# Kernel optimization log

Measured on AMD Instinct MI355X. Metric: run time of the kernel, lower is better.

The kernel has to match this reference:

```python
import math
import jax, jax.numpy as jnp
import numpy as np

B, T, C = 4, 2048, 1024

def setup_inputs() -> dict:
    key = jax.random.key(0)
    k1, k2 = jax.random.split(key)
    x = jax.random.normal(k1, (B, T, C), dtype=jnp.float32)
    W_kqv = jax.random.normal(k2, (C, 3 * C), dtype=jnp.float32) * 0.02
    return {"x": x, "W_kqv": W_kqv}

def reference(x, W_kqv):
    Bq, Tq, Cq = x.shape
    qkv = jnp.einsum('btc,cd->btd', x, W_kqv)            # [B,T,3C]
    q, k, v = jnp.split(qkv, 3, axis=2)                   # each [B,T,C]
    # scaled scores: note scale is 1/sqrt(n_embed), matching the source
    attn = jnp.einsum('btc,bsc->bts', q, k) / math.sqrt(Cq)  # [B,T,T]
    mask = jnp.tril(jnp.ones((Tq, Tq), dtype=bool))
    attn = jnp.where(mask, attn, -jnp.inf)
    attn = jax.nn.softmax(attn, axis=-1)
    y = jnp.einsum('bts,bsc->btc', attn, v)               # [B,T,C]
    return y
```

## Files before the change

### kernel.cpp

```cpp
#include <hip/hip_runtime.h>

typedef unsigned short u16;
typedef __bf16 bf16x8 __attribute__((ext_vector_type(8)));
typedef float f32x4 __attribute__((ext_vector_type(4)));

#define Bb 4
#define Tt 2048
#define Cc 1024

#define GLOAD_LDS16(g, l)                                                     \
  __builtin_amdgcn_global_load_lds(                                           \
      (const __attribute__((address_space(1))) void*)(g),                     \
      (__attribute__((address_space(3))) void*)(l), 16, 0, 0)

#define WAITV8 asm volatile("s_waitcnt vmcnt(8)" ::: "memory")
#define WAITV0 asm volatile("s_waitcnt vmcnt(0)" ::: "memory")

__device__ inline u16 f2bf(float f) {
  unsigned u = __builtin_bit_cast(unsigned, f);
  unsigned r = u + 0x7fffu + ((u >> 16) & 1u);
  return (u16)(r >> 16);
}

__global__ __launch_bounds__(256) void cast_f32_bf16_vec4(
    const float* __restrict__ in, u16* __restrict__ out, int n4) {
  int i = blockIdx.x * 256 + threadIdx.x;
  if (i >= n4) return;
  float4 v = reinterpret_cast<const float4*>(in)[i];
  ushort4 o;
  o.x = f2bf(v.x); o.y = f2bf(v.y); o.z = f2bf(v.z); o.w = f2bf(v.w);
  reinterpret_cast<ushort4*>(out)[i] = o;
}

__global__ __launch_bounds__(256) void zero_f32(float* __restrict__ p, int n) {
  int i = blockIdx.x * 256 + threadIdx.x;
  if (i < n) p[i] = 0.f;
}

__global__ __launch_bounds__(256) void transpose_cast_w(
    const float* __restrict__ W, u16* __restrict__ Wt) {
  __shared__ float tile[32][33];
  int n0 = blockIdx.x * 32;
  int k0 = blockIdx.y * 32;
  int tx = threadIdx.x;
  int ty = threadIdx.y;
#pragma unroll
  for (int i = 0; i < 4; i++)
    tile[ty + i * 8][tx] = W[(size_t)(k0 + ty + i * 8) * 3072 + n0 + tx];
  __syncthreads();
#pragma unroll
  for (int i = 0; i < 4; i++)
    Wt[(size_t)(n0 + ty + i * 8) * 1024 + k0 + tx] = f2bf(tile[tx][ty + i * 8]);
}

__device__ __forceinline__ void stage_unit(const u16* __restrict__ G, int ld,
                                           u16* lds_unit, int tid) {
#pragma unroll
  for (int j = 0; j < 2; j++) {
    int u = j * 8192 + tid * 16;
    int l = u ^ (((u >> 7) & 7) << 4);
    GLOAD_LDS16(G + (size_t)(l >> 6) * ld + ((l & 63) >> 1), lds_unit + (u >> 1));
  }
}

__device__ __forceinline__ bf16x8 lds_frag(const u16* unit, int row, int fq) {
  int off = row * 64 + fq * 16;
  off ^= ((off >> 7) & 7) << 4;
  return *reinterpret_cast<const bf16x8*>(
      reinterpret_cast<const char*>(unit) + off);
}

__device__ __forceinline__ void stageA256(const u16* __restrict__ G,
                                          u16* unit, int tid) {
#pragma unroll
  for (int j = 0; j < 4; j++) {
    int u = j * 4096 + tid * 16;
    int l = u ^ (((u >> 7) & 7) << 4);
    GLOAD_LDS16(G + (size_t)(l >> 6) * Cc + ((l & 63) >> 1), unit + (u >> 1));
  }
}
__device__ __forceinline__ void stageB256(const u16* __restrict__ G,
                                          u16* unit, int tid) {
#pragma unroll
  for (int j = 0; j < 2; j++) {
    int u = j * 4096 + tid * 16;
    int l = u ^ (((u >> 7) & 7) << 4);
    GLOAD_LDS16(G + (size_t)(l >> 6) * Cc + ((l & 63) >> 1), unit + (u >> 1));
  }
}

__global__ __launch_bounds__(256, 3) void gemm_qkv_256x128(
    const u16* __restrict__ A0, const u16* __restrict__ B0,
    u16* __restrict__ qO, u16* __restrict__ kO, u16* __restrict__ vTO) {
  const int NT = Cc / 32;
  int bx = blockIdx.x, by = blockIdx.y;
  const u16* A = A0 + (size_t)by * 256 * Cc;
  const u16* Bt = B0 + (size_t)bx * 128 * Cc;

  __shared__ __attribute__((aligned(16))) u16 ldsA[2][8192];
  __shared__ __attribute__((aligned(16))) u16 ldsB[2][4096];

  int tid = threadIdx.x;
  int lane = tid & 63, w = tid >> 6;
  int wm = (w >> 1) * 128, wn = (w & 1) * 64;
  int fr = lane & 15, fq = lane >> 4;

  f32x4 acc[8][4] = {};

  stageA256(A, ldsA[0], tid);
  stageB256(Bt, ldsB[0], tid);
  WAITV0;
  __builtin_amdgcn_s_barrier();

  for (int t = 0; t < NT; ++t) {
    int par = t & 1, parn = par ^ 1;
    if (t + 1 < NT) {
      stageA256(A + (t + 1) * 32, ldsA[parn], tid);
      stageB256(Bt + (t + 1) * 32, ldsB[parn], tid);
    }
    bf16x8 a[4], b[4];
#pragma unroll
    for (int ni = 0; ni < 4; ni++)
      b[ni] = lds_frag(ldsB[par], wn + ni * 16 + fr, fq);
#pragma unroll
    for (int mi = 0; mi < 4; mi++)
      a[mi] = lds_frag(ldsA[par], wm + mi * 16 + fr, fq);
    __builtin_amdgcn_s_setprio(1);
#pragma unroll
    for (int mi = 0; mi < 4; mi++)
#pragma unroll
      for (int ni = 0; ni < 4; ni++)
        acc[mi][ni] = __builtin_amdgcn_mfma_f32_16x16x32_bf16(a[mi], b[ni], acc[mi][ni], 0, 0, 0);
    __builtin_amdgcn_s_setprio(0);
#pragma unroll
    for (int mi = 0; mi < 4; mi++)
      a[mi] = lds_frag(ldsA[par], wm + 64 + mi * 16 + fr, fq);
    __builtin_amdgcn_s_setprio(1);
#pragma unroll
    for (int mi = 0; mi < 4; mi++)
#pragma unroll
      for (int ni = 0; ni < 4; ni++)
        acc[4 + mi][ni] = __builtin_amdgcn_mfma_f32_16x16x32_bf16(a[mi], b[ni], acc[4 + mi][ni], 0, 0, 0);
    __builtin_amdgcn_s_setprio(0);
    if (t + 1 < NT) WAITV0;
    __builtin_amdgcn_s_barrier();
  }

#pragma unroll
  for (int mi = 0; mi < 8; mi++) {
#pragma unroll
    for (int ni = 0; ni < 4; ni++) {
#pragma unroll
      for (int r = 0; r < 4; r++) {
        int m = by * 256 + wm + mi * 16 + fq * 4 + r;
        int n = bx * 128 + wn + ni * 16 + fr;
        u16 hv = f2bf(acc[mi][ni][r]);
        int seg = n >> 10, cn = n & 1023;
        int b = m >> 11, tt = m & 2047;
        if (seg == 0)
          qO[(((size_t)(b * Tt + tt)) << 10) + cn] = hv;
        else if (seg == 1)
          kO[(((size_t)(b * Tt + tt)) << 10) + cn] = hv;
        else
          vTO[((size_t)(b * Cc + cn)) * Tt + tt] = hv;
      }
    }
  }
}

template <int MODE>
__global__ __launch_bounds__(512, 2) void gemm256(
    const u16* __restrict__ A0, const u16* __restrict__ B0,
    size_t sAbatch, size_t sBbatch,
    u16* __restrict__ EO, float* __restrict__ rowsum) {
  const int lda = Cc, ldb = Cc, NT = Cc / 64;
  int bx = blockIdx.x, by = blockIdx.y, bz = blockIdx.z;
  if (MODE == 1 && bx > by) return;

  const u16* A = A0 + (size_t)bz * sAbatch + (size_t)by * 256 * lda;
  const u16* Bt = B0 + (size_t)bz * sBbatch + (size_t)bx * 256 * ldb;

  __shared__ __attribute__((aligned(16))) u16 lds[4][2][8192];

  int tid = threadIdx.x;
  int lane = tid & 63, w = tid >> 6;
  int wm = (w >> 2) * 128, wn = (w & 3) * 64;
  int fr = lane & 15, fq = lane >> 4;

  f32x4 acc[8][4] = {};

  stage_unit(A + 0, lda, &lds[0][0][0], tid);
  stage_unit(Bt + 0, ldb, &lds[2][0][0], tid);
  stage_unit(A + 32, lda, &lds[1][0][0], tid);
  stage_unit(Bt + 32, ldb, &lds[3][0][0], tid);
  stage_unit(A + 64, lda, &lds[0][1][0], tid);
  stage_unit(Bt + 64, ldb, &lds[2][1][0], tid);
  WAITV8;
  __builtin_amdgcn_s_barrier();

  for (int t = 0; t < NT; ++t) {
    int par = t & 1;
    int parn = par ^ 1;
    bool st1 = (t + 1 < NT);
    bool st2 = (t + 2 < NT);
    bool tail = (t >= NT - 2);
    bf16x8 a[4], b[4];

#pragma unroll
    for (int mi = 0; mi < 4; mi++)
      a[mi] = lds_frag(&lds[0][par][0], wm + mi * 16 + fr, fq);
#pragma unroll
    for (int ni = 0; ni < 4; ni++)
      b[ni] = lds_frag(&lds[2][par][0], wn + ni * 16 + fr, fq);
    if (st1) stage_unit(A + (t + 1) * 64 + 32, lda, &lds[1][parn][0], tid);
    __builtin_amdgcn_s_barrier();
    __builtin_amdgcn_s_setprio(1);
#pragma unroll
    for (int mi = 0; mi < 4; mi++)
#pragma unroll
      for (int ni = 0; ni < 4; ni++)
        acc[mi][ni] = __builtin_amdgcn_mfma_f32_16x16x32_bf16(a[mi], b[ni], acc[mi][ni], 0, 0, 0);
    __builtin_amdgcn_s_setprio(0);
    __builtin_amdgcn_s_barrier();

#pragma unroll
    for (int mi = 0; mi < 4; mi++)
      a[mi] = lds_frag(&lds[0][par][0], wm + 64 + mi * 16 + fr, fq);
    if (st1) stage_unit(Bt + (t + 1) * 64 + 32, ldb, &lds[3][parn][0], tid);
    __builtin_amdgcn_s_barrier();
    __builtin_amdgcn_s_setprio(1);
#pragma unroll
    for (int mi = 0; mi < 4; mi++)
#pragma unroll
      for (int ni = 0; ni < 4; ni++)
        acc[4 + mi][ni] = __builtin_amdgcn_mfma_f32_16x16x32_bf16(a[mi], b[ni], acc[4 + mi][ni], 0, 0, 0);
    __builtin_amdgcn_s_setprio(0);
    if (tail) { WAITV0; } else { WAITV8; }
    __builtin_amdgcn_s_barrier();

#pragma unroll
    for (int mi = 0; mi < 4; mi++)
      a[mi] = lds_frag(&lds[1][par][0], wm + mi * 16 + fr, fq);
#pragma unroll
    for (int ni = 0; ni < 4; ni++)
      b[ni] = lds_frag(&lds[3][par][0], wn + ni * 16 + fr, fq);
    if (st2) stage_unit(A + (t + 2) * 64, lda, &lds[0][par][0], tid);
    __builtin_amdgcn_s_barrier();
    __builtin_amdgcn_s_setprio(1);
#pragma unroll
    for (int mi = 0; mi < 4; mi++)
#pragma unroll
      for (int ni = 0; ni < 4; ni++)
        acc[mi][ni] = __builtin_amdgcn_mfma_f32_16x16x32_bf16(a[mi], b[ni], acc[mi][ni], 0, 0, 0);
    __builtin_amdgcn_s_setprio(0);
    __builtin_amdgcn_s_barrier();

#pragma unroll
    for (int mi = 0; mi < 4; mi++)
      a[mi] = lds_frag(&lds[1][par][0], wm + 64 + mi * 16 + fr, fq);
    if (st2) stage_unit(Bt + (t + 2) * 64, ldb, &lds[2][par][0], tid);
    __builtin_amdgcn_s_barrier();
    __builtin_amdgcn_s_setprio(1);
#pragma unroll
    for (int mi = 0; mi < 4; mi++)
#pragma unroll
      for (int ni = 0; ni < 4; ni++)
        acc[4 + mi][ni] = __builtin_amdgcn_mfma_f32_16x16x32_bf16(a[mi], b[ni], acc[4 + mi][ni], 0, 0, 0);
    __builtin_amdgcn_s_setprio(0);
    if (tail) { WAITV0; } else { WAITV8; }
    __builtin_amdgcn_s_barrier();
  }

  {
    float rpart[8][4];
#pragma unroll
    for (int mi = 0; mi < 8; mi++)
#pragma unroll
      for (int r = 0; r < 4; r++) rpart[mi][r] = 0.f;
#pragma unroll
    for (int mi = 0; mi < 8; mi++) {
#pragma unroll
      for (int ni = 0; ni < 4; ni++) {
#pragma unroll
        for (int r = 0; r < 4; r++) {
          int m = by * 256 + wm + mi * 16 + fq * 4 + r;
          int n = bx * 256 + wn + ni * 16 + fr;
          float e = 0.f;
          if (n <= m) e = __expf(fminf(acc[mi][ni][r] * 0.03125f, 30.f));
          EO[((size_t)bz * Tt + m) * Tt + n] = f2bf(e);
          rpart[mi][r] += e;
        }
      }
    }
#pragma unroll
    for (int mi = 0; mi < 8; mi++) {
#pragma unroll
      for (int r = 0; r < 4; r++) {
        float v = rpart[mi][r];
        v += __shfl_xor(v, 1);
        v += __shfl_xor(v, 2);
        v += __shfl_xor(v, 4);
        v += __shfl_xor(v, 8);
        if (fr == 0) {
          int m = by * 256 + wm + mi * 16 + fq * 4 + r;
          atomicAdd(&rowsum[(size_t)bz * Tt + m], v);
        }
      }
    }
  }
}

__global__ __launch_bounds__(256) void gemm_bt_pv(
    const u16* __restrict__ A0, const u16* __restrict__ B0,
    size_t sAbatch, size_t sBbatch,
    int K, int lda, int ldb, const float* __restrict__ rowsum,
    float* __restrict__ YO) {
  int bx = blockIdx.x, by = blockIdx.y, bz = blockIdx.z;

  const u16* A = A0 + (size_t)bz * sAbatch + (size_t)by * 128 * lda;
  const u16* Bt = B0 + (size_t)bz * sBbatch + (size_t)bx * 128 * ldb;
  int kEnd = min(K, (by + 1) * 128);

  __shared__ __attribute__((aligned(16))) u16 As[128 * 32];
  __shared__ __attribute__((aligned(16))) u16 Bs[128 * 32];

  int tid = threadIdx.x;
  int lane = tid & 63, w = tid >> 6;
  int wr = (w >> 1) * 64, wc = (w & 1) * 64;
  int row16 = lane & 15, kq = (lane >> 4) * 8;

  int r0 = w * 16 + (lane >> 2);
  int c0 = (lane & 3) * 8;

  f32x4 acc[4][4] = {};

  for (int kt = 0; kt < kEnd; kt += 32) {
    const u16* Ag = A + (size_t)r0 * lda + kt + c0;
    const u16* Bg = Bt + (size_t)r0 * ldb + kt + c0;
    GLOAD_LDS16(Ag, &As[w * 512]);
    GLOAD_LDS16(Ag + (size_t)64 * lda, &As[2048 + w * 512]);
    GLOAD_LDS16(Bg, &Bs[w * 512]);
    GLOAD_LDS16(Bg + (size_t)64 * ldb, &Bs[2048 + w * 512]);
    __syncthreads();

    bf16x8 a[4], b[4];
#pragma unroll
    for (int m = 0; m < 4; m++)
      a[m] = *reinterpret_cast<const bf16x8*>(&As[(wr + m * 16 + row16) * 32 + kq]);
#pragma unroll
    for (int n = 0; n < 4; n++)
      b[n] = *reinterpret_cast<const bf16x8*>(&Bs[(wc + n * 16 + row16) * 32 + kq]);
#pragma unroll
    for (int m = 0; m < 4; m++)
#pragma unroll
      for (int n = 0; n < 4; n++)
        acc[m][n] = __builtin_amdgcn_mfma_f32_16x16x32_bf16(a[m], b[n], acc[m][n], 0, 0, 0);
    __syncthreads();
  }

  int colf = lane & 15, rbase = (lane >> 4) * 4;
#pragma unroll
  for (int i = 0; i < 4; i++) {
#pragma unroll
    for (int r = 0; r < 4; r++) {
      int m = by * 128 + wr + i * 16 + rbase + r;
      float inv = 1.0f / rowsum[(size_t)bz * Tt + m];
#pragma unroll
      for (int j = 0; j < 4; j++) {
        int n = bx * 128 + wc + j * 16 + colf;
        YO[((size_t)bz * Tt + m) * Cc + n] = acc[i][j][r] * inv;
      }
    }
  }
}

extern "C" void kernel_launch(void* const* d_in, const int* in_sizes, int n_in,
                              void* d_out, int out_size, void* d_ws, size_t ws_size,
                              hipStream_t stream) {
  const float* x = (const float*)d_in[0];
  const float* W = (const float*)d_in[1];
  float* Y = (float*)d_out;

  char* ws = (char*)d_ws;
  size_t off = 0;
  auto carve = [&](size_t bytes) -> void* {
    void* p = ws + off;
    off += (bytes + 255) & ~(size_t)255;
    return p;
  };
  u16* xb = (u16*)carve((size_t)Bb * Tt * Cc * 2);
  u16* wt = (u16*)carve((size_t)3 * Cc * Cc * 2);
  u16* qb = (u16*)carve((size_t)Bb * Tt * Cc * 2);
  u16* kb = (u16*)carve((size_t)Bb * Tt * Cc * 2);
  u16* vT = (u16*)carve((size_t)Bb * Cc * Tt * 2);
  u16* E = (u16*)carve((size_t)Bb * Tt * Tt * 2);
  float* rowsum = (float*)carve((size_t)Bb * Tt * 4);

  cast_f32_bf16_vec4<<<(Bb * Tt * Cc / 4 + 255) / 256, 256, 0, stream>>>(
      x, xb, Bb * Tt * Cc / 4);
  zero_f32<<<(Bb * Tt + 255) / 256, 256, 0, stream>>>(rowsum, Bb * Tt);
  transpose_cast_w<<<dim3(96, 32), dim3(32, 8), 0, stream>>>(W, wt);
  gemm_qkv_256x128<<<dim3(24, 32), 256, 0, stream>>>(xb, wt, qb, kb, vT);
  gemm256<1><<<dim3(8, 8, 4), 512, 0, stream>>>(
      qb, kb, (size_t)Tt * Cc, (size_t)Tt * Cc, E, rowsum);
  gemm_bt_pv<<<dim3(8, 16, 4), 256, 0, stream>>>(
      E, vT, (size_t)Tt * Tt, (size_t)Cc * Tt, Tt, Tt, Tt, rowsum, Y);
}
```

Baseline: 306.7 us.

## Retile QKV GEMM to 256x384 tiles with 8 waves and deeper staged pipeline

The QKV projection GEMM moves from 256x128 tiles with 4 waves and a 2-deep buffer to 256x384 tiles with 8 waves. K steps grow to 64, split into two 32-wide sub-buffers that are prefetched with interleaved barriers and partial vmcnt waits. The grid shrinks to 256 blocks, exactly one per CU, which cuts redundant A loads and raises arithmetic intensity. In exchange, occupancy drops to one block per CU and the accumulator register count grows. The templated score GEMM is de-templated without any change to its behaviour.

```diff
diff --git a/kernel.cpp b/kernel.cpp
--- a/kernel.cpp
+++ b/kernel.cpp
@@ -13,6 +13,7 @@
       (const __attribute__((address_space(1))) void*)(g),                     \
       (__attribute__((address_space(3))) void*)(l), 16, 0, 0)
 
+#define WAITV10 asm volatile("s_waitcnt vmcnt(10)" ::: "memory")
 #define WAITV8 asm volatile("s_waitcnt vmcnt(8)" ::: "memory")
 #define WAITV0 asm volatile("s_waitcnt vmcnt(0)" ::: "memory")
 
@@ -53,13 +54,22 @@
     Wt[(size_t)(n0 + ty + i * 8) * 1024 + k0 + tx] = f2bf(tile[tx][ty + i * 8]);
 }
 
-__device__ __forceinline__ void stage_unit(const u16* __restrict__ G, int ld,
-                                           u16* lds_unit, int tid) {
+__device__ __forceinline__ void stage_unitA(const u16* __restrict__ G,
+                                            u16* lds_unit, int tid) {
 #pragma unroll
   for (int j = 0; j < 2; j++) {
     int u = j * 8192 + tid * 16;
     int l = u ^ (((u >> 7) & 7) << 4);
-    GLOAD_LDS16(G + (size_t)(l >> 6) * ld + ((l & 63) >> 1), lds_unit + (u >> 1));
+    GLOAD_LDS16(G + (size_t)(l >> 6) * Cc + ((l & 63) >> 1), lds_unit + (u >> 1));
+  }
+}
+__device__ __forceinline__ void stage_unitB3(const u16* __restrict__ G,
+                                             u16* lds_unit, int tid) {
+#pragma unroll
+  for (int j = 0; j < 3; j++) {
+    int u = j * 8192 + tid * 16;
+    int l = u ^ (((u >> 7) & 7) << 4);
+    GLOAD_LDS16(G + (size_t)(l >> 6) * Cc + ((l & 63) >> 1), lds_unit + (u >> 1));
   }
 }
 
@@ -70,90 +80,113 @@
       reinterpret_cast<const char*>(unit) + off);
 }
 
-__device__ __forceinline__ void stageA256(const u16* __restrict__ G,
-                                          u16* unit, int tid) {
-#pragma unroll
-  for (int j = 0; j < 4; j++) {
-    int u = j * 4096 + tid * 16;
-    int l = u ^ (((u >> 7) & 7) << 4);
-    GLOAD_LDS16(G + (size_t)(l >> 6) * Cc + ((l & 63) >> 1), unit + (u >> 1));
-  }
-}
-__device__ __forceinline__ void stageB256(const u16* __restrict__ G,
-                                          u16* unit, int tid) {
-#pragma unroll
-  for (int j = 0; j < 2; j++) {
-    int u = j * 4096 + tid * 16;
-    int l = u ^ (((u >> 7) & 7) << 4);
-    GLOAD_LDS16(G + (size_t)(l >> 6) * Cc + ((l & 63) >> 1), unit + (u >> 1));
-  }
-}
-
-__global__ __launch_bounds__(256, 3) void gemm_qkv_256x128(
+__global__ __launch_bounds__(512, 1) void gemm_qkv_384(
     const u16* __restrict__ A0, const u16* __restrict__ B0,
     u16* __restrict__ qO, u16* __restrict__ kO, u16* __restrict__ vTO) {
-  const int NT = Cc / 32;
+  const int NT = Cc / 64;
   int bx = blockIdx.x, by = blockIdx.y;
   const u16* A = A0 + (size_t)by * 256 * Cc;
-  const u16* Bt = B0 + (size_t)bx * 128 * Cc;
-
-  __shared__ __attribute__((aligned(16))) u16 ldsA[2][8192];
-  __shared__ __attribute__((aligned(16))) u16 ldsB[2][4096];
+  const u16* Bt = B0 + (size_t)bx * 384 * Cc;
+
+  __shared__ __attribute__((aligned(16))) u16 ldsA[2][2][8192];
+  __shared__ __attribute__((aligned(16))) u16 ldsB[2][2][12288];
 
   int tid = threadIdx.x;
   int lane = tid & 63, w = tid >> 6;
-  int wm = (w >> 1) * 128, wn = (w & 1) * 64;
+  int wm = (w >> 2) * 128, wn = (w & 3) * 96;
   int fr = lane & 15, fq = lane >> 4;
 
-  f32x4 acc[8][4] = {};
-
-  stageA256(A, ldsA[0], tid);
-  stageB256(Bt, ldsB[0], tid);
-  WAITV0;
+  f32x4 acc[8][6] = {};
+
+  stage_unitA(A + 0, &ldsA[0][0][0], tid);
+  stage_unitB3(Bt + 0, &ldsB[0][0][0], tid);
+  stage_unitA(A + 32, &ldsA[1][0][0], tid);
+  stage_unitB3(Bt + 32, &ldsB[1][0][0], tid);
+  stage_unitA(A + 64, &ldsA[0][1][0], tid);
+  stage_unitB3(Bt + 64, &ldsB[0][1][0], tid);
+  WAITV10;
   __builtin_amdgcn_s_barrier();
 
   for (int t = 0; t < NT; ++t) {
     int par = t & 1, parn = par ^ 1;
-    if (t + 1 < NT) {
-      stageA256(A + (t + 1) * 32, ldsA[parn], tid);
-      stageB256(Bt + (t + 1) * 32, ldsB[parn], tid);
-    }
-    bf16x8 a[4], b[4];
-#pragma unroll
-    for (int ni = 0; ni < 4; ni++)
-      b[ni] = lds_frag(ldsB[par], wn + ni * 16 + fr, fq);
-#pragma unroll
-    for (int mi = 0; mi < 4; mi++)
-      a[mi] = lds_frag(ldsA[par], wm + mi * 16 + fr, fq);
-    __builtin_amdgcn_s_setprio(1);
-#pragma unroll
-    for (int mi = 0; mi < 4; mi++)
-#pragma unroll
-      for (int ni = 0; ni < 4; ni++)
+    bool st1 = (t + 1 < NT);
+    bool st2 = (t + 2 < NT);
+    bool tail = (t >= NT - 2);
+    bf16x8 a[4], b[6];
+
+#pragma unroll
+    for (int mi = 0; mi < 4; mi++)
+      a[mi] = lds_frag(&ldsA[0][par][0], wm + mi * 16 + fr, fq);
+#pragma unroll
+    for (int ni = 0; ni < 6; ni++)
+      b[ni] = lds_frag(&ldsB[0][par][0], wn + ni * 16 + fr, fq);
+    if (st1) stage_unitA(A + (t + 1) * 64 + 32, &ldsA[1][parn][0], tid);
+    __builtin_amdgcn_s_barrier();
+    __builtin_amdgcn_s_setprio(1);
+#pragma unroll
+    for (int mi = 0; mi < 4; mi++)
+#pragma unroll
+      for (int ni = 0; ni < 6; ni++)
         acc[mi][ni] = __builtin_amdgcn_mfma_f32_16x16x32_bf16(a[mi], b[ni], acc[mi][ni], 0, 0, 0);
     __builtin_amdgcn_s_setprio(0);
-#pragma unroll
-    for (int mi = 0; mi < 4; mi++)
-      a[mi] = lds_frag(ldsA[par], wm + 64 + mi * 16 + fr, fq);
-    __builtin_amdgcn_s_setprio(1);
-#pragma unroll
-    for (int mi = 0; mi < 4; mi++)
-#pragma unroll
-      for (int ni = 0; ni < 4; ni++)
+    __builtin_amdgcn_s_barrier();
+
+#pragma unroll
+    for (int mi = 0; mi < 4; mi++)
+      a[mi] = lds_frag(&ldsA[0][par][0], wm + 64 + mi * 16 + fr, fq);
+    if (st1) stage_unitB3(Bt + (t + 1) * 64 + 32, &ldsB[1][parn][0], tid);
+    __builtin_amdgcn_s_barrier();
+    __builtin_amdgcn_s_setprio(1);
+#pragma unroll
+    for (int mi = 0; mi < 4; mi++)
+#pragma unroll
+      for (int ni = 0; ni < 6; ni++)
         acc[4 + mi][ni] = __builtin_amdgcn_mfma_f32_16x16x32_bf16(a[mi], b[ni], acc[4 + mi][ni], 0, 0, 0);
     __builtin_amdgcn_s_setprio(0);
-    if (t + 1 < NT) WAITV0;
+    if (tail) { WAITV0; } else { WAITV10; }
+    __builtin_amdgcn_s_barrier();
+
+#pragma unroll
+    for (int mi = 0; mi < 4; mi++)
+      a[mi] = lds_frag(&ldsA[1][par][0], wm + mi * 16 + fr, fq);
+#pragma unroll
+    for (int ni = 0; ni < 6; ni++)
+      b[ni] = lds_frag(&ldsB[1][par][0], wn + ni * 16 + fr, fq);
+    if (st2) stage_unitA(A + (t + 2) * 64, &ldsA[0][par][0], tid);
+    __builtin_amdgcn_s_barrier();
+    __builtin_amdgcn_s_setprio(1);
+#pragma unroll
+    for (int mi = 0; mi < 4; mi++)
+#pragma unroll
+      for (int ni = 0; ni < 6; ni++)
+        acc[mi][ni] = __builtin_amdgcn_mfma_f32_16x16x32_bf16(a[mi], b[ni], acc[mi][ni], 0, 0, 0);
+    __builtin_amdgcn_s_setprio(0);
+    __builtin_amdgcn_s_barrier();
+
+#pragma unroll
+    for (int mi = 0; mi < 4; mi++)
+      a[mi] = lds_frag(&ldsA[1][par][0], wm + 64 + mi * 16 + fr, fq);
+    if (st2) stage_unitB3(Bt + (t + 2) * 64, &ldsB[0][par][0], tid);
+    __builtin_amdgcn_s_barrier();
+    __builtin_amdgcn_s_setprio(1);
+#pragma unroll
+    for (int mi = 0; mi < 4; mi++)
+#pragma unroll
+      for (int ni = 0; ni < 6; ni++)
+        acc[4 + mi][ni] = __builtin_amdgcn_mfma_f32_16x16x32_bf16(a[mi], b[ni], acc[4 + mi][ni], 0, 0, 0);
+    __builtin_amdgcn_s_setprio(0);
+    if (tail) { WAITV0; } else { WAITV10; }
     __builtin_amdgcn_s_barrier();
   }
 
 #pragma unroll
   for (int mi = 0; mi < 8; mi++) {
 #pragma unroll
-    for (int ni = 0; ni < 4; ni++) {
+    for (int ni = 0; ni < 6; ni++) {
 #pragma unroll
       for (int r = 0; r < 4; r++) {
         int m = by * 256 + wm + mi * 16 + fq * 4 + r;
-        int n = bx * 128 + wn + ni * 16 + fr;
+        int n = bx * 384 + wn + ni * 16 + fr;
         u16 hv = f2bf(acc[mi][ni][r]);
         int seg = n >> 10, cn = n & 1023;
         int b = m >> 11, tt = m & 2047;
@@ -168,14 +201,23 @@
   }
 }
 
-template <int MODE>
-__global__ __launch_bounds__(512, 2) void gemm256(
+__device__ __forceinline__ void stage_unit(const u16* __restrict__ G, int ld,
+                                           u16* lds_unit, int tid) {
+#pragma unroll
+  for (int j = 0; j < 2; j++) {
+    int u = j * 8192 + tid * 16;
+    int l = u ^ (((u >> 7) & 7) << 4);
+    GLOAD_LDS16(G + (size_t)(l >> 6) * ld + ((l & 63) >> 1), lds_unit + (u >> 1));
+  }
+}
+
+__global__ __launch_bounds__(512, 2) void gemm256_e(
     const u16* __restrict__ A0, const u16* __restrict__ B0,
     size_t sAbatch, size_t sBbatch,
     u16* __restrict__ EO, float* __restrict__ rowsum) {
   const int lda = Cc, ldb = Cc, NT = Cc / 64;
   int bx = blockIdx.x, by = blockIdx.y, bz = blockIdx.z;
-  if (MODE == 1 && bx > by) return;
+  if (bx > by) return;
 
   const u16* A = A0 + (size_t)bz * sAbatch + (size_t)by * 256 * lda;
   const u16* Bt = B0 + (size_t)bz * sBbatch + (size_t)bx * 256 * ldb;
@@ -400,8 +442,8 @@
       x, xb, Bb * Tt * Cc / 4);
   zero_f32<<<(Bb * Tt + 255) / 256, 256, 0, stream>>>(rowsum, Bb * Tt);
   transpose_cast_w<<<dim3(96, 32), dim3(32, 8), 0, stream>>>(W, wt);
-  gemm_qkv_256x128<<<dim3(24, 32), 256, 0, stream>>>(xb, wt, qb, kb, vT);
-  gemm256<1><<<dim3(8, 8, 4), 512, 0, stream>>>(
+  gemm_qkv_384<<<dim3(8, 32), 512, 0, stream>>>(xb, wt, qb, kb, vT);
+  gemm256_e<<<dim3(8, 8, 4), 512, 0, stream>>>(
       qb, kb, (size_t)Tt * Cc, (size_t)Tt * Cc, E, rowsum);
   gemm_bt_pv<<<dim3(8, 16, 4), 256, 0, stream>>>(
       E, vT, (size_t)Tt * Tt, (size_t)Cc * Tt, Tt, Tt, Tt, rowsum, Y);
```

New measurement: 330.1 us. 1.08x slower.
